# Optimization experiments

Hardware: AMD Instinct MI355X
Metric: run time of the kernel (lower is better)

The kernel has to match this reference:

```python
import jax, jax.numpy as jnp
import numpy as np

NBINS = 128
LOGSCALE = False


def setup_inputs() -> dict:
    key = jax.random.key(0)
    X = jax.random.normal(key, (2048, 32768), dtype=jnp.float32)
    return {"X": X}


def reference(X) -> jnp.ndarray:
    # Flatten all non-leading dims (mirrors X.view(len(X), -1))
    X = X.reshape(X.shape[0], -1)
    ns = X.shape[1]
    nfreqs = 2 * (NBINS - 1) + 1          # window length (255)
    hop = nfreqs // 2
    starts = jnp.arange(0, ns - nfreqs + 1, hop)          # [nwin]
    idx = starts[:, None] + jnp.arange(nfreqs)[None, :]    # [nwin, nfreqs]
    W = X[:, idx]                          # [ntrials, nwin, nfreqs] gathered windows
    # One batched rfft + fused |.|^2 and mean over windows (Welch average)
    S = jnp.mean(jnp.abs(jnp.fft.rfft(W, axis=-1)) ** 2, axis=1)  # [ntrials, NBINS]
    if LOGSCALE:
        S = jnp.log10(S)
    return S
```

## Files before the change

kernel.cpp:

```cpp
#include <hip/hip_runtime.h>
#include <hip/hip_bf16.h>

#define NS     32768
#define NROWS  2048
#define HOP    127
#define NW     257
#define NB     128
#define WTILE  16
#define NT     17
#define TWOPI_255 0.02463994236f

typedef _Float16 f16;
typedef __attribute__((ext_vector_type(2))) _Float16 f16x2;
typedef __attribute__((ext_vector_type(4))) _Float16 f16x4;
typedef __attribute__((ext_vector_type(8))) _Float16 f16x8;
typedef __attribute__((ext_vector_type(4))) float f32x4;

__device__ inline f32x4 load4u(const char* p) {
    f32x4 v;
    __builtin_memcpy(&v, p, 16);
    return v;
}

__global__ __launch_bounds__(256)
void basis_kernel(f16* __restrict__ bt) {
    const int t  = blockIdx.x * 256 + threadIdx.x;
    const int fi = t >> 6;
    const int l  = t & 63;
    const int cq = fi >> 3;
    const int nt = (fi >> 2) & 1;
    const int kk = fi & 3;
    const int is_sin = cq >> 2;
    const int f  = (cq & 3) * 32 + nt * 16 + (l & 15);
    int m = (f * (kk * 32 + (l >> 4) * 8)) % 255;
    f16x8 v;
    #pragma unroll
    for (int j = 0; j < 8; ++j) {
        const float ang = (float)m * TWOPI_255;
        v[j] = (f16)(is_sin ? __sinf(ang) : __cosf(ang));
        m += f; if (m >= 255) m -= 255;
    }
    *(f16x8*)(bt + (size_t)t * 8) = v;
}

__global__ __launch_bounds__(512, 6)
void psd_kernel(const float* __restrict__ X, const f16* __restrict__ bt,
                float* __restrict__ out) {
    const int row  = blockIdx.x;
    const int tid  = threadIdx.x;
    const int lane = tid & 63;
    const int cq   = tid >> 6;
    const int r16  = lane & 15;
    const int kg   = lane >> 4;
    const int is_sin = cq >> 2;

    __shared__ alignas(16) f16 atile[2][WTILE * 256];
    __shared__ float scol[256];

    const char* __restrict__ xrow = (const char*)(X + (size_t)row * NS);

    const int sw  = tid >> 5;
    const int sq  = tid & 31;
    const int sk0 = sq * 4;

    const uint voff_f = (uint)((sw * HOP + sk0) * 4);
    const uint voff_r = (uint)((sw * HOP + 252 - sk0) * 4);

    f32x4 fv = load4u(xrow + voff_f);
    f32x4 rv = load4u(xrow + voff_r);

    f16x8 bfrag[2][4];
    {
        const char* bp = (const char*)bt + (uint)(cq * 8192 + lane * 16);
        #pragma unroll
        for (int nt = 0; nt < 2; ++nt)
            #pragma unroll
            for (int kk = 0; kk < 4; ++kk)
                bfrag[nt][kk] = *(const f16x8*)(bp + (uint)((nt * 4 + kk) * 1024));
    }

    char* const lds = (char*)&atile[0][0];

    const uint swz  = (uint)((sw & 7) << 4);
    const uint wr_p = ((uint)(sw * 512 + sq * 8)) ^ swz;
    const uint wr_m = ((uint)(sw * 512 + sq * 8 + 256)) ^ swz;
    const uint rswz = (uint)((r16 & 7) << 4);
    uint rd[4];
    #pragma unroll
    for (int kk = 0; kk < 4; ++kk)
        rd[kk] = ((uint)(r16 * 512 + is_sin * 256 + kg * 16 + kk * 64)) ^ rswz;

    auto fold_write = [&](char* wp, bool valid) {
        const f16x2 fp01 = __builtin_bit_cast(f16x2, __builtin_amdgcn_cvt_pkrtz(fv[0], fv[1]));
        const f16x2 fp23 = __builtin_bit_cast(f16x2, __builtin_amdgcn_cvt_pkrtz(fv[2], fv[3]));
        const f16x2 rp01 = __builtin_bit_cast(f16x2, __builtin_amdgcn_cvt_pkrtz(rv[3], rv[2]));
        const f16x2 rp23 = __builtin_bit_cast(f16x2, __builtin_amdgcn_cvt_pkrtz(rv[1], rv[0]));
        const f16x2 yp01 = fp01 + rp01, yp23 = fp23 + rp23;
        const f16x2 ym01 = fp01 - rp01, ym23 = fp23 - rp23;
        f16x4 h0, h1;
        h0[0] = yp01[0]; h0[1] = yp01[1]; h0[2] = yp23[0]; h0[3] = yp23[1];
        h1[0] = ym01[0]; h1[1] = ym01[1]; h1[2] = ym23[0]; h1[3] = ym23[1];
        if (sq == 0) { h0[0] = (f16)fv[0]; h1[0] = (f16)0.0f; }
        if (!valid) {
            #pragma unroll
            for (int j = 0; j < 4; ++j) { h0[j] = (f16)0.0f; h1[j] = (f16)0.0f; }
        }
        *(f16x4*)(wp + wr_p) = h0;
        *(f16x4*)(wp + wr_m) = h1;
    };

    fold_write(lds, true);
    {
        const uint base = (uint)(WTILE * HOP * 4);
        fv = load4u(xrow + (voff_f + base));
        rv = load4u(xrow + (voff_r + base));
    }
    asm volatile("s_waitcnt lgkmcnt(0)" ::: "memory");
    __builtin_amdgcn_s_barrier();
    asm volatile("" ::: "memory");

    float ssum0 = 0.f, ssum1 = 0.f;
    const uint vclamp = (uint)((NS - 4) * 4);

    for (int mt = 0; mt < NT; ++mt) {
        const char* ap = lds + ((mt & 1) << 13);

        f32x4 acc0 = {0,0,0,0}, acc1 = {0,0,0,0};
        __builtin_amdgcn_s_setprio(1);
        #pragma unroll
        for (int kk = 0; kk < 4; ++kk) {
            const f16x8 af = *(const f16x8*)(ap + rd[kk]);
            acc0 = __builtin_amdgcn_mfma_f32_16x16x32_f16(af, bfrag[0][kk], acc0, 0, 0, 0);
            acc1 = __builtin_amdgcn_mfma_f32_16x16x32_f16(af, bfrag[1][kk], acc1, 0, 0, 0);
        }
        __builtin_amdgcn_s_setprio(0);
        #pragma unroll
        for (int r = 0; r < 4; ++r) {
            ssum0 += acc0[r] * acc0[r];
            ssum1 += acc1[r] * acc1[r];
        }

        if (mt < NT - 1) {
            char* wp = lds + (((mt + 1) & 1) << 13);
            const bool valid = (mt != 15) || (sw == 0);
            fold_write(wp, valid);
            if (mt < NT - 2) {
                const uint base = (uint)((mt + 2) * WTILE * HOP * 4);
                fv = load4u(xrow + min(voff_f + base, vclamp));
                rv = load4u(xrow + min(voff_r + base, vclamp));
            }
            asm volatile("s_waitcnt lgkmcnt(0)" ::: "memory");
            __builtin_amdgcn_s_barrier();
            asm volatile("" ::: "memory");
        }
    }

    {
        float v = ssum0;
        v += __shfl_xor(v, 16, 64);
        v += __shfl_xor(v, 32, 64);
        if (kg == 0) scol[is_sin * 128 + (cq & 3) * 32 + r16] = v;
        float w = ssum1;
        w += __shfl_xor(w, 16, 64);
        w += __shfl_xor(w, 32, 64);
        if (kg == 0) scol[is_sin * 128 + (cq & 3) * 32 + 16 + r16] = w;
    }
    __syncthreads();
    if (tid < NB) {
        out[(size_t)row * NB + tid] = (scol[tid] + scol[tid + NB]) * (1.0f / 257.0f);
    }
}

extern "C" void kernel_launch(void* const* d_in, const int* in_sizes, int n_in,
                              void* d_out, int out_size, void* d_ws, size_t ws_size,
                              hipStream_t stream) {
    const float* X = (const float*)d_in[0];
    float* out = (float*)d_out;
    f16* bt = (f16*)d_ws;
    (void)in_sizes; (void)n_in; (void)ws_size; (void)out_size;
    basis_kernel<<<dim3(16), dim3(256), 0, stream>>>(bt);
    psd_kernel<<<dim3(NROWS), dim3(512), 0, stream>>>(X, bt, out);
}
```

Baseline: 53.51 us.

## Double window tile per step and reassign waves to 2x2 M/N split

```diff
diff --git a/kernel.cpp b/kernel.cpp
--- a/kernel.cpp
+++ b/kernel.cpp
@@ -6,13 +6,12 @@
 #define HOP    127
 #define NW     257
 #define NB     128
-#define WTILE  16
-#define NT     17
+#define WT2    32
+#define NT2    9
 #define TWOPI_255 0.02463994236f
 
 typedef _Float16 f16;
 typedef __attribute__((ext_vector_type(2))) _Float16 f16x2;
-typedef __attribute__((ext_vector_type(4))) _Float16 f16x4;
 typedef __attribute__((ext_vector_type(8))) _Float16 f16x8;
 typedef __attribute__((ext_vector_type(4))) float f32x4;
 
@@ -43,7 +42,7 @@
     *(f16x8*)(bt + (size_t)t * 8) = v;
 }
 
-__global__ __launch_bounds__(512, 6)
+__global__ __launch_bounds__(512, 3)
 void psd_kernel(const float* __restrict__ X, const f16* __restrict__ bt,
                 float* __restrict__ out) {
     const int row  = blockIdx.x;
@@ -52,102 +51,121 @@
     const int cq   = tid >> 6;
     const int r16  = lane & 15;
     const int kg   = lane >> 4;
-    const int is_sin = cq >> 2;
-
-    __shared__ alignas(16) f16 atile[2][WTILE * 256];
-    __shared__ float scol[256];
+    const int mg   = cq >> 2;
+    const int hs   = (cq >> 1) & 1;
+    const int ng   = cq & 1;
+
+    __shared__ alignas(16) f16 atile[2][WT2 * 256];
+    __shared__ float scol[2][256];
 
     const char* __restrict__ xrow = (const char*)(X + (size_t)row * NS);
 
-    const int sw  = tid >> 5;
-    const int sq  = tid & 31;
-    const int sk0 = sq * 4;
-
-    const uint voff_f = (uint)((sw * HOP + sk0) * 4);
-    const uint voff_r = (uint)((sw * HOP + 252 - sk0) * 4);
-
-    f32x4 fv = load4u(xrow + voff_f);
-    f32x4 rv = load4u(xrow + voff_r);
-
-    f16x8 bfrag[2][4];
+    const int sw2 = tid >> 4;
+    const int sq2 = tid & 15;
+
+    const uint voff_f = (uint)((sw2 * HOP + sq2 * 8) * 4);
+    const uint voff_r = (uint)((sw2 * HOP + 248 - sq2 * 8) * 4);
+    const uint vclamp = (uint)((NS - 4) * 4);
+
+    f32x4 fva = load4u(xrow + voff_f);
+    f32x4 fvb = load4u(xrow + voff_f + 16);
+    f32x4 rva = load4u(xrow + voff_r);
+    f32x4 rvb = load4u(xrow + voff_r + 16);
+
+    f16x8 bfrag[4][4];
     {
-        const char* bp = (const char*)bt + (uint)(cq * 8192 + lane * 16);
-        #pragma unroll
-        for (int nt = 0; nt < 2; ++nt)
+        const char* bp = (const char*)bt + (uint)(lane * 16);
+        #pragma unroll
+        for (int nt = 0; nt < 4; ++nt) {
+            const int fi = (hs * 4 + ng * 2 + (nt >> 1)) * 8 + (nt & 1) * 4;
             #pragma unroll
             for (int kk = 0; kk < 4; ++kk)
-                bfrag[nt][kk] = *(const f16x8*)(bp + (uint)((nt * 4 + kk) * 1024));
+                bfrag[nt][kk] = *(const f16x8*)(bp + (uint)((fi + kk) * 1024));
+        }
     }
 
     char* const lds = (char*)&atile[0][0];
 
-    const uint swz  = (uint)((sw & 7) << 4);
-    const uint wr_p = ((uint)(sw * 512 + sq * 8)) ^ swz;
-    const uint wr_m = ((uint)(sw * 512 + sq * 8 + 256)) ^ swz;
-    const uint rswz = (uint)((r16 & 7) << 4);
+    const uint wr_p = ((uint)(sw2 * 512 + sq2 * 16)) ^ ((uint)((sw2 & 7) << 4));
+    const uint wr_m = wr_p + 256;
+    const int  arow = mg * 16 + r16;
     uint rd[4];
     #pragma unroll
     for (int kk = 0; kk < 4; ++kk)
-        rd[kk] = ((uint)(r16 * 512 + is_sin * 256 + kg * 16 + kk * 64)) ^ rswz;
+        rd[kk] = ((uint)(arow * 512 + hs * 256 + kg * 16 + kk * 64))
+               ^ ((uint)((arow & 7) << 4));
 
     auto fold_write = [&](char* wp, bool valid) {
-        const f16x2 fp01 = __builtin_bit_cast(f16x2, __builtin_amdgcn_cvt_pkrtz(fv[0], fv[1]));
-        const f16x2 fp23 = __builtin_bit_cast(f16x2, __builtin_amdgcn_cvt_pkrtz(fv[2], fv[3]));
-        const f16x2 rp01 = __builtin_bit_cast(f16x2, __builtin_amdgcn_cvt_pkrtz(rv[3], rv[2]));
-        const f16x2 rp23 = __builtin_bit_cast(f16x2, __builtin_amdgcn_cvt_pkrtz(rv[1], rv[0]));
-        const f16x2 yp01 = fp01 + rp01, yp23 = fp23 + rp23;
-        const f16x2 ym01 = fp01 - rp01, ym23 = fp23 - rp23;
-        f16x4 h0, h1;
-        h0[0] = yp01[0]; h0[1] = yp01[1]; h0[2] = yp23[0]; h0[3] = yp23[1];
-        h1[0] = ym01[0]; h1[1] = ym01[1]; h1[2] = ym23[0]; h1[3] = ym23[1];
-        if (sq == 0) { h0[0] = (f16)fv[0]; h1[0] = (f16)0.0f; }
+        f16x8 h0, h1;
+        #pragma unroll
+        for (int q = 0; q < 4; ++q) {
+            const int j0 = 2 * q, j1 = 2 * q + 1;
+            const float f0 = (j0 < 4) ? fva[j0] : fvb[j0 - 4];
+            const float f1 = (j1 < 4) ? fva[j1] : fvb[j1 - 4];
+            const float r0 = (j0 < 4) ? rvb[3 - j0] : rva[7 - j0];
+            const float r1 = (j1 < 4) ? rvb[3 - j1] : rva[7 - j1];
+            const f16x2 fp = __builtin_bit_cast(f16x2, __builtin_amdgcn_cvt_pkrtz(f0, f1));
+            const f16x2 rp = __builtin_bit_cast(f16x2, __builtin_amdgcn_cvt_pkrtz(r0, r1));
+            const f16x2 s = fp + rp;
+            const f16x2 d = fp - rp;
+            h0[j0] = s[0]; h0[j1] = s[1];
+            h1[j0] = d[0]; h1[j1] = d[1];
+        }
+        if (sq2 == 0) { h0[0] = (f16)fva[0]; h1[0] = (f16)0.0f; }
         if (!valid) {
             #pragma unroll
-            for (int j = 0; j < 4; ++j) { h0[j] = (f16)0.0f; h1[j] = (f16)0.0f; }
-        }
-        *(f16x4*)(wp + wr_p) = h0;
-        *(f16x4*)(wp + wr_m) = h1;
+            for (int j = 0; j < 8; ++j) { h0[j] = (f16)0.0f; h1[j] = (f16)0.0f; }
+        }
+        *(f16x8*)(wp + wr_p) = h0;
+        *(f16x8*)(wp + wr_m) = h1;
     };
 
     fold_write(lds, true);
     {
-        const uint base = (uint)(WTILE * HOP * 4);
-        fv = load4u(xrow + (voff_f + base));
-        rv = load4u(xrow + (voff_r + base));
+        const uint tb = (uint)(WT2 * HOP * 4);
+        fva = load4u(xrow + (voff_f + tb));
+        fvb = load4u(xrow + (voff_f + tb + 16));
+        rva = load4u(xrow + (voff_r + tb));
+        rvb = load4u(xrow + (voff_r + tb + 16));
     }
     asm volatile("s_waitcnt lgkmcnt(0)" ::: "memory");
     __builtin_amdgcn_s_barrier();
     asm volatile("" ::: "memory");
 
-    float ssum0 = 0.f, ssum1 = 0.f;
-    const uint vclamp = (uint)((NS - 4) * 4);
-
-    for (int mt = 0; mt < NT; ++mt) {
-        const char* ap = lds + ((mt & 1) << 13);
-
-        f32x4 acc0 = {0,0,0,0}, acc1 = {0,0,0,0};
+    float ssum[4] = {0.f, 0.f, 0.f, 0.f};
+
+    for (int mt = 0; mt < NT2; ++mt) {
+        const char* ap = lds + ((mt & 1) << 14);
+
+        f32x4 acc0 = {0,0,0,0}, acc1 = {0,0,0,0}, acc2 = {0,0,0,0}, acc3 = {0,0,0,0};
         __builtin_amdgcn_s_setprio(1);
         #pragma unroll
         for (int kk = 0; kk < 4; ++kk) {
             const f16x8 af = *(const f16x8*)(ap + rd[kk]);
             acc0 = __builtin_amdgcn_mfma_f32_16x16x32_f16(af, bfrag[0][kk], acc0, 0, 0, 0);
             acc1 = __builtin_amdgcn_mfma_f32_16x16x32_f16(af, bfrag[1][kk], acc1, 0, 0, 0);
+            acc2 = __builtin_amdgcn_mfma_f32_16x16x32_f16(af, bfrag[2][kk], acc2, 0, 0, 0);
+            acc3 = __builtin_amdgcn_mfma_f32_16x16x32_f16(af, bfrag[3][kk], acc3, 0, 0, 0);
         }
         __builtin_amdgcn_s_setprio(0);
         #pragma unroll
         for (int r = 0; r < 4; ++r) {
-            ssum0 += acc0[r] * acc0[r];
-            ssum1 += acc1[r] * acc1[r];
-        }
-
-        if (mt < NT - 1) {
-            char* wp = lds + (((mt + 1) & 1) << 13);
-            const bool valid = (mt != 15) || (sw == 0);
+            ssum[0] += acc0[r] * acc0[r];
+            ssum[1] += acc1[r] * acc1[r];
+            ssum[2] += acc2[r] * acc2[r];
+            ssum[3] += acc3[r] * acc3[r];
+        }
+
+        if (mt < NT2 - 1) {
+            char* wp = lds + (((mt + 1) & 1) << 14);
+            const bool valid = (mt != NT2 - 2) || (sw2 == 0);
             fold_write(wp, valid);
-            if (mt < NT - 2) {
-                const uint base = (uint)((mt + 2) * WTILE * HOP * 4);
-                fv = load4u(xrow + min(voff_f + base, vclamp));
-                rv = load4u(xrow + min(voff_r + base, vclamp));
+            if (mt < NT2 - 2) {
+                const uint tb = (uint)((mt + 2) * WT2 * HOP * 4);
+                fva = load4u(xrow + min(voff_f + tb,      vclamp));
+                fvb = load4u(xrow + min(voff_f + tb + 16, vclamp));
+                rva = load4u(xrow + min(voff_r + tb,      vclamp));
+                rvb = load4u(xrow + min(voff_r + tb + 16, vclamp));
             }
             asm volatile("s_waitcnt lgkmcnt(0)" ::: "memory");
             __builtin_amdgcn_s_barrier();
@@ -155,19 +173,18 @@
         }
     }
 
-    {
-        float v = ssum0;
+    #pragma unroll
+    for (int nt = 0; nt < 4; ++nt) {
+        float v = ssum[nt];
         v += __shfl_xor(v, 16, 64);
         v += __shfl_xor(v, 32, 64);
-        if (kg == 0) scol[is_sin * 128 + (cq & 3) * 32 + r16] = v;
-        float w = ssum1;
-        w += __shfl_xor(w, 16, 64);
-        w += __shfl_xor(w, 32, 64);
-        if (kg == 0) scol[is_sin * 128 + (cq & 3) * 32 + 16 + r16] = w;
+        if (kg == 0) scol[mg][hs * 128 + ng * 64 + nt * 16 + r16] = v;
     }
     __syncthreads();
     if (tid < NB) {
-        out[(size_t)row * NB + tid] = (scol[tid] + scol[tid + NB]) * (1.0f / 257.0f);
+        const float s = scol[0][tid] + scol[0][tid + NB]
+                      + scol[1][tid] + scol[1][tid + NB];
+        out[(size_t)row * NB + tid] = s * (1.0f / 257.0f);
     }
 }
 
```

Result: slower. 126.4 us (+136.3%).

## Quad-buffer the LDS window tiles and barrier every other tile

Applied to the files above, without the earlier changes.

```diff
diff --git a/kernel.cpp b/kernel.cpp
--- a/kernel.cpp
+++ b/kernel.cpp
@@ -54,17 +54,17 @@
     const int kg   = lane >> 4;
     const int is_sin = cq >> 2;
 
-    __shared__ alignas(16) f16 atile[2][WTILE * 256];
+    __shared__ alignas(16) f16 atile[4][WTILE * 256];
     __shared__ float scol[256];
 
     const char* __restrict__ xrow = (const char*)(X + (size_t)row * NS);
 
     const int sw  = tid >> 5;
     const int sq  = tid & 31;
-    const int sk0 = sq * 4;
 
-    const uint voff_f = (uint)((sw * HOP + sk0) * 4);
-    const uint voff_r = (uint)((sw * HOP + 252 - sk0) * 4);
+    const uint voff_f = (uint)((sw * HOP + sq * 4) * 4);
+    const uint voff_r = (uint)((sw * HOP + 252 - sq * 4) * 4);
+    const uint vclamp = (uint)((NS - 4) * 4);
 
     f32x4 fv = load4u(xrow + voff_f);
     f32x4 rv = load4u(xrow + voff_r);
@@ -109,21 +109,26 @@
         *(f16x4*)(wp + wr_m) = h1;
     };
 
-    fold_write(lds, true);
+    fold_write(lds + (0 << 13), true);
     {
-        const uint base = (uint)(WTILE * HOP * 4);
-        fv = load4u(xrow + (voff_f + base));
-        rv = load4u(xrow + (voff_r + base));
+        const uint tb = (uint)(1 * WTILE * HOP * 4);
+        fv = load4u(xrow + (voff_f + tb));
+        rv = load4u(xrow + (voff_r + tb));
+    }
+    fold_write(lds + (1 << 13), true);
+    {
+        const uint tb = (uint)(2 * WTILE * HOP * 4);
+        fv = load4u(xrow + (voff_f + tb));
+        rv = load4u(xrow + (voff_r + tb));
     }
     asm volatile("s_waitcnt lgkmcnt(0)" ::: "memory");
     __builtin_amdgcn_s_barrier();
     asm volatile("" ::: "memory");
 
     float ssum0 = 0.f, ssum1 = 0.f;
-    const uint vclamp = (uint)((NS - 4) * 4);
 
     for (int mt = 0; mt < NT; ++mt) {
-        const char* ap = lds + ((mt & 1) << 13);
+        const char* ap = lds + ((mt & 3) << 13);
 
         f32x4 acc0 = {0,0,0,0}, acc1 = {0,0,0,0};
         __builtin_amdgcn_s_setprio(1);
@@ -140,15 +145,17 @@
             ssum1 += acc1[r] * acc1[r];
         }
 
-        if (mt < NT - 1) {
-            char* wp = lds + (((mt + 1) & 1) << 13);
-            const bool valid = (mt != 15) || (sw == 0);
+        if (mt + 2 < NT) {
+            char* wp = lds + (((mt + 2) & 3) << 13);
+            const bool valid = (mt + 2 != 16) || (sw == 0);
             fold_write(wp, valid);
-            if (mt < NT - 2) {
-                const uint base = (uint)((mt + 2) * WTILE * HOP * 4);
-                fv = load4u(xrow + min(voff_f + base, vclamp));
-                rv = load4u(xrow + min(voff_r + base, vclamp));
+            if (mt + 3 < NT) {
+                const uint tb = (uint)((mt + 3) * WTILE * HOP * 4);
+                fv = load4u(xrow + min(voff_f + tb, vclamp));
+                rv = load4u(xrow + min(voff_r + tb, vclamp));
             }
+        }
+        if (mt & 1) {
             asm volatile("s_waitcnt lgkmcnt(0)" ::: "memory");
             __builtin_amdgcn_s_barrier();
             asm volatile("" ::: "memory");
```

Measured after the change: 53.52 us. No clear change (+0.0%).
